# Kernel optimization log

Measured on AMD Instinct MI355X. Metric: run time of the kernel, lower is better.

## Reference

```python
import jax, jax.numpy as jnp
import numpy as np

B, S, H = 1, 2048, 4096
NH, NKV, D = 32, 8, 128
ROPE_THETA = 10000.0


def _rotate_half(x):
    half = x.shape[-1] // 2
    return jnp.concatenate([-x[..., half:], x[..., :half]], axis=-1)


def _rope_cos_sin(position_ids, dim, theta):
    inv_freq = 1.0 / (theta ** (jnp.arange(0, dim, 2, dtype=jnp.float32) / dim))  # [D/2]
    freqs = position_ids.astype(jnp.float32)[..., None] * inv_freq  # [B,S,D/2]
    emb = jnp.concatenate([freqs, freqs], axis=-1)  # [B,S,D]
    return jnp.cos(emb)[:, None], jnp.sin(emb)[:, None]  # [B,1,S,D]


def setup_inputs() -> dict:
    key = jax.random.key(0)
    k1, k2, k3 = jax.random.split(key, 3)
    hidden_states = jax.random.normal(k1, (B, S, H), dtype=jnp.float32)
    # fused QKV weight: columns = [NH*D | NKV*D | NKV*D]
    w_qkv = jax.random.normal(k2, (H, (NH + 2 * NKV) * D), dtype=jnp.float32) * (1.0 / np.sqrt(H))
    w_o = jax.random.normal(k3, (NH * D, H), dtype=jnp.float32) * (1.0 / np.sqrt(NH * D))
    attention_mask = jnp.tril(jnp.ones((S, S), dtype=bool))[None, None]  # causal [1,1,S,S]
    position_ids = jnp.arange(S, dtype=jnp.int64 if jax.config.jax_enable_x64 else jnp.int32)[None, :]
    return {"hidden_states": hidden_states, "w_qkv": w_qkv, "w_o": w_o,
            "attention_mask": attention_mask, "position_ids": position_ids}


def reference(hidden_states, w_qkv, w_o, attention_mask, position_ids):
    bsz, q_len, _ = hidden_states.shape
    qk_scale = 1.0 / np.sqrt(D)

    # fused QKV projection
    qkv = jnp.einsum('bsh,hc->bsc', hidden_states, w_qkv)
    q = qkv[..., : NH * D].reshape(bsz, q_len, NH, D).transpose(0, 2, 1, 3)        # [B,NH,S,D]
    k = qkv[..., NH * D: (NH + NKV) * D].reshape(bsz, q_len, NKV, D).transpose(0, 2, 1, 3)
    v = qkv[..., (NH + NKV) * D:].reshape(bsz, q_len, NKV, D).transpose(0, 2, 1, 3)

    # RoPE
    cos, sin = _rope_cos_sin(position_ids, D, ROPE_THETA)
    q = q * cos + _rotate_half(q) * sin
    k = k * cos + _rotate_half(k) * sin

    # GQA expand kv heads
    groups = NH // NKV
    k = jnp.repeat(k, groups, axis=1)  # [B,NH,S,D]
    v = jnp.repeat(v, groups, axis=1)

    # causal masked attention (eager path, matches scaled_qk + softmax(fp32))
    scores = jnp.einsum('bhqd,bhkd->bhqk', q, k) * qk_scale
    scores = jnp.where(attention_mask, scores, jnp.finfo(scores.dtype).min)
    probs = jax.nn.softmax(scores.astype(jnp.float32), axis=-1).astype(q.dtype)
    attn = jnp.einsum('bhqk,bhkd->bhqd', probs, v)  # [B,NH,S,D]

    # merge heads + output projection
    attn = attn.transpose(0, 2, 1, 3).reshape(bsz, q_len, NH * D)
    return jnp.einsum('bsd,dh->bsh', attn, w_o)
```

## Files before the change

kernel.cpp:

```cpp
#include <hip/hip_runtime.h>
#include <cstdint>
#include <cstddef>


#define DEV __device__ __forceinline__

typedef __attribute__((ext_vector_type(4))) float  f32x4;
typedef __attribute__((ext_vector_type(4))) short  short4v;
typedef __attribute__((ext_vector_type(8))) short  short8;
typedef __attribute__((ext_vector_type(8))) __bf16 bf16x8;

DEV short f32_to_bf16(float x) {
  union { float f; uint32_t u; } v; v.f = x;
  uint32_t r = v.u + 0x7fffu + ((v.u >> 16) & 1u);
  return (short)(r >> 16);
}

union frag_u { short4v h[2]; bf16x8 v; short s[8]; uint32_t u[4]; };
DEV bf16x8 comb(short4v lo, short4v hi) { frag_u u; u.h[0] = lo; u.h[1] = hi; return u.v; }

DEV uint32_t pack2bf_trunc(float a, float b) {
  union { float f; uint32_t u; } x, y; x.f = a; y.f = b;
  return (x.u >> 16) | (y.u & 0xFFFF0000u);
}

DEV f32x4 MFMA(bf16x8 a, bf16x8 b, f32x4 c) {
  return __builtin_amdgcn_mfma_f32_16x16x32_bf16(a, b, c, 0, 0, 0);
}

typedef __attribute__((address_space(1))) void* gas1p;
typedef __attribute__((address_space(3))) void* as3p;
DEV void gld16(const void* g, void* l) {
  __builtin_amdgcn_global_load_lds((gas1p)g, (as3p)l, 16, 0, 0);
}

#define VMCNT(n) asm volatile("s_waitcnt vmcnt(" #n ")" ::: "memory")


__global__ __launch_bounds__(256) void k_cvt_bf16(const float* __restrict__ x,
                                                  short* __restrict__ y, int n4) {
  int i = blockIdx.x * 256 + threadIdx.x;
  int stride = gridDim.x * 256;
  for (; i < n4; i += stride) {
    f32x4 v = ((const f32x4*)x)[i];
    short4v o;
    o[0] = f32_to_bf16(v[0]); o[1] = f32_to_bf16(v[1]);
    o[2] = f32_to_bf16(v[2]); o[3] = f32_to_bf16(v[3]);
    ((short4v*)y)[i] = o;
  }
}

__global__ __launch_bounds__(256) void k_transpose64(const float* __restrict__ src,
                                                     short* __restrict__ dst,
                                                     int R, int C, int stride) {
  __shared__ float tile[64][65];
  const int c0 = blockIdx.x * 64, r0 = blockIdx.y * 64;
  const int t = threadIdx.x;
  const int lr = t >> 4;
  const int lc = (t & 15) * 4;
  #pragma unroll
  for (int p = 0; p < 4; ++p) {
    const int r = p * 16 + lr;
    f32x4 v = *(const f32x4*)(src + (long)(r0 + r) * stride + c0 + lc);
    tile[r][lc] = v[0]; tile[r][lc + 1] = v[1]; tile[r][lc + 2] = v[2]; tile[r][lc + 3] = v[3];
  }
  __syncthreads();
  #pragma unroll
  for (int p = 0; p < 4; ++p) {
    const int c = p * 16 + lr;
    short4v o;
    o[0] = f32_to_bf16(tile[lc][c]);     o[1] = f32_to_bf16(tile[lc + 1][c]);
    o[2] = f32_to_bf16(tile[lc + 2][c]); o[3] = f32_to_bf16(tile[lc + 3][c]);
    *(short4v*)(dst + (long)(c0 + c) * R + r0 + lc) = o;
  }
}

__global__ __launch_bounds__(256) void k_vtrans64(const float* __restrict__ C1,
                                                  short* __restrict__ Vt) {
  __shared__ float tile[64][65];
  const int s0 = blockIdx.x * 64, d0 = blockIdx.y * 64, z = blockIdx.z;
  const int t = threadIdx.x;
  const int lr = t >> 4;
  const int lc = (t & 15) * 4;
  const float* src = C1 + 5120 + z * 128;
  #pragma unroll
  for (int p = 0; p < 4; ++p) {
    const int r = p * 16 + lr;
    f32x4 v = *(const f32x4*)(src + (long)(s0 + r) * 6144 + d0 + lc);
    tile[r][lc] = v[0]; tile[r][lc + 1] = v[1]; tile[r][lc + 2] = v[2]; tile[r][lc + 3] = v[3];
  }
  __syncthreads();
  short* dst = Vt + (long)z * 128 * 2048;
  #pragma unroll
  for (int p = 0; p < 4; ++p) {
    const int d = p * 16 + lr;
    short4v o;
    o[0] = f32_to_bf16(tile[lc][d]);     o[1] = f32_to_bf16(tile[lc + 1][d]);
    o[2] = f32_to_bf16(tile[lc + 2][d]); o[3] = f32_to_bf16(tile[lc + 3][d]);
    *(short4v*)(dst + (long)(d0 + d) * 2048 + s0 + lc) = o;
  }
}

__global__ __launch_bounds__(256) void k_rope_pack(const float* __restrict__ C1,
                                                   short* __restrict__ Qh,
                                                   short* __restrict__ Kh) {
  __shared__ float cs[64], sn[64];
  const int s = blockIdx.x, t = threadIdx.x;
  if (t < 64) {
    float inv = powf(10000.0f, -(float)t * (1.0f / 64.0f));
    float a = (float)s * inv;
    cs[t] = cosf(a);
    sn[t] = sinf(a);
  }
  __syncthreads();
  const float* row = C1 + (long)s * 6144;
  for (int i = t; i < 2048; i += 256) {
    int hh = i >> 6, j = i & 63;
    float c = cs[j], ss = sn[j];
    float x0 = row[hh * 128 + j], x1 = row[hh * 128 + j + 64];
    long o = ((long)hh * 2048 + s) * 128 + j;
    Qh[o]      = f32_to_bf16(x0 * c - x1 * ss);
    Qh[o + 64] = f32_to_bf16(x1 * c + x0 * ss);
  }
  for (int i = t; i < 512; i += 256) {
    int hh = i >> 6, j = i & 63;
    float c = cs[j], ss = sn[j];
    float x0 = row[4096 + hh * 128 + j], x1 = row[4096 + hh * 128 + j + 64];
    long o = ((long)hh * 2048 + s) * 128 + j;
    Kh[o]      = f32_to_bf16(x0 * c - x1 * ss);
    Kh[o + 64] = f32_to_bf16(x1 * c + x0 * ss);
  }
}


template<int MR>
DEV void gemm8p_engine(const short* __restrict__ A, const short* __restrict__ Bt,
                       float* __restrict__ Cp, int N, int K,
                       char* __restrict__ AsB, char* __restrict__ BsB) {
  constexpr int BM = MR * 32;
  const int tid = threadIdx.x;
  const int lane = tid & 63;
  const int w = tid >> 6;
  const int wm = w >> 2, wn = w & 3;
  const int wr = wm * (MR * 16);
  const int wc = wn * 64;
  const int g = lane >> 4, r16 = lane & 15;
  const long m0 = (long)blockIdx.y * BM;
  const long n0 = (long)blockIdx.x * 256;
  const int l8 = lane >> 3, l7 = lane & 7;
  const int sslot = l7 ^ l8;

  f32x4 acc[MR][4] = {};
  const int NT = K >> 6;

  auto stageA = [&](int h, int kt, int bufn) {
    #pragma unroll
    for (int s = 0; s < BM / 128; ++s) {
      const int rb = h * (BM / 2) + s * 64 + w * 8;
      gld16(A + (m0 + rb + l8) * (long)K + kt * 64 + sslot * 8,
            AsB + ((size_t)bufn * BM + rb) * 128);
    }
  };
  auto stageB = [&](int h, int kt, int bufn) {
    #pragma unroll
    for (int s = 0; s < 2; ++s) {
      const int rb = h * 128 + s * 64 + w * 8;
      gld16(Bt + (n0 + rb + l8) * (long)K + kt * 64 + sslot * 8,
            BsB + ((size_t)bufn * 256 + rb) * 128);
    }
  };

  bf16x8 a[MR / 2][2], b0[2][2], b1[2][2];

  #define LDA_HALF(h, buf) { _Pragma("unroll") for (int m = 0; m < MR/2; ++m) \
      _Pragma("unroll") for (int kk = 0; kk < 2; ++kk) { \
        const int row = wr + ((h) * (MR/2) + m) * 16 + r16; \
        const int slot = ((kk << 2) | g) ^ (r16 & 7); \
        a[m][kk] = *(const bf16x8*)(AsB + ((size_t)(buf) * BM + row) * 128 + slot * 16); } }
  #define LDB_HALF(dst, h, buf) { _Pragma("unroll") for (int n = 0; n < 2; ++n) \
      _Pragma("unroll") for (int kk = 0; kk < 2; ++kk) { \
        const int row = wc + ((h) * 2 + n) * 16 + r16; \
        const int slot = ((kk << 2) | g) ^ (r16 & 7); \
        dst[n][kk] = *(const bf16x8*)(BsB + ((size_t)(buf) * 256 + row) * 128 + slot * 16); } }
  #define QUADQ(mh, nh, bb) { __builtin_amdgcn_s_setprio(1); \
      _Pragma("unroll") for (int m = 0; m < MR/2; ++m) \
      _Pragma("unroll") for (int n = 0; n < 2; ++n) \
      _Pragma("unroll") for (int kk = 0; kk < 2; ++kk) \
        acc[(mh) * (MR/2) + m][(nh) * 2 + n] = \
          MFMA(a[m][kk], bb[n][kk], acc[(mh) * (MR/2) + m][(nh) * 2 + n]); \
      __builtin_amdgcn_s_setprio(0); }

  stageA(0, 0, 0); stageB(0, 0, 0); stageB(1, 0, 0); stageA(1, 0, 0);
  VMCNT(4);
  __builtin_amdgcn_s_barrier();

  for (int t = 0; t < NT - 1; ++t) {
    const int buf = t & 1, bufn = buf ^ 1, tn = t + 1;
    LDA_HALF(0, buf); LDB_HALF(b0, 0, buf);
    stageA(0, tn, bufn);
    __builtin_amdgcn_s_barrier();
    QUADQ(0, 0, b0);
    VMCNT(4);
    __builtin_amdgcn_s_barrier();
    LDB_HALF(b1, 1, buf);
    stageB(0, tn, bufn);
    __builtin_amdgcn_s_barrier();
    QUADQ(0, 1, b1);
    VMCNT(4);
    __builtin_amdgcn_s_barrier();
    LDA_HALF(1, buf);
    stageB(1, tn, bufn);
    __builtin_amdgcn_s_barrier();
    QUADQ(1, 1, b1);
    __builtin_amdgcn_s_barrier();
    stageA(1, tn, bufn);
    QUADQ(1, 0, b0);
    VMCNT(4);
    __builtin_amdgcn_s_barrier();
  }
  {
    const int buf = (NT - 1) & 1;
    LDA_HALF(0, buf); LDB_HALF(b0, 0, buf);
    __builtin_amdgcn_s_barrier();
    QUADQ(0, 0, b0);
    VMCNT(2);
    __builtin_amdgcn_s_barrier();
    LDB_HALF(b1, 1, buf);
    __builtin_amdgcn_s_barrier();
    QUADQ(0, 1, b1);
    VMCNT(0);
    __builtin_amdgcn_s_barrier();
    LDA_HALF(1, buf);
    __builtin_amdgcn_s_barrier();
    QUADQ(1, 1, b1);
    QUADQ(1, 0, b0);
  }
  #undef LDA_HALF
  #undef LDB_HALF
  #undef QUADQ

  #pragma unroll
  for (int m = 0; m < MR; ++m) {
    #pragma unroll
    for (int n = 0; n < 4; ++n) {
      const long col = n0 + wc + n * 16 + r16;
      #pragma unroll
      for (int j = 0; j < 4; ++j) {
        const long row = m0 + wr + m * 16 + g * 4 + j;
        Cp[row * N + col] = acc[m][n][j];
      }
    }
  }
}

__global__ __launch_bounds__(512, 2) void k_gemm1_8p(const short* __restrict__ A,
                                                     const short* __restrict__ Bt,
                                                     float* __restrict__ C, int N, int K) {
  __shared__ short As[2][256][64];
  __shared__ short Bs[2][256][64];
  gemm8p_engine<8>(A, Bt, C, N, K, (char*)&As[0][0][0], (char*)&Bs[0][0][0]);
}


template<int OUT_BF16>
__global__ __launch_bounds__(256, 2) void k_gemm128(const short* __restrict__ A,
                                                    const short* __restrict__ Bt,
                                                    void* __restrict__ Cp,
                                                    int M, int N, int K) {
  __shared__ short As[2][128][64];
  __shared__ short Bs[2][128][64];
  const int tid = threadIdx.x;
  const int lane = tid & 63;
  const int w = tid >> 6;
  const int wr = (w >> 1) * 64;
  const int wc = (w & 1) * 64;
  const int g = lane >> 4, r16 = lane & 15;
  const long m0 = (long)blockIdx.y * 128;
  const long n0 = (long)blockIdx.x * 128;
  const int l8 = lane >> 3, l7 = lane & 7;
  const int sslot = l7 ^ l8;

  f32x4 acc[4][4] = {};
  const int NT = K >> 6;

  auto stageTile = [&](int kt, int buf) {
    #pragma unroll
    for (int L = 0; L < 4; ++L) {
      const int rb = (w * 4 + L) * 8;
      gld16(A  + (m0 + rb + l8) * (long)K + kt * 64 + sslot * 8, (char*)&As[buf][rb][0]);
      gld16(Bt + (n0 + rb + l8) * (long)K + kt * 64 + sslot * 8, (char*)&Bs[buf][rb][0]);
    }
  };
  auto ldA = [&](int m, int kk, int buf) -> bf16x8 {
    const int row = wr + m * 16 + r16;
    const int slot = ((kk << 2) | g) ^ (r16 & 7);
    return *(const bf16x8*)((const char*)&As[buf][0][0] + row * 128 + slot * 16);
  };
  auto ldB = [&](int n, int kk, int buf) -> bf16x8 {
    const int row = wc + n * 16 + r16;
    const int slot = ((kk << 2) | g) ^ (r16 & 7);
    return *(const bf16x8*)((const char*)&Bs[buf][0][0] + row * 128 + slot * 16);
  };

  stageTile(0, 0);
  __syncthreads();

  for (int t = 0; t < NT; ++t) {
    const int buf = t & 1;
    if (t + 1 < NT) stageTile(t + 1, buf ^ 1);

    bf16x8 a[2][2], b[2][2];
    #pragma unroll
    for (int mh = 0; mh < 2; ++mh) {
      #pragma unroll
      for (int m = 0; m < 2; ++m)
        #pragma unroll
        for (int kk = 0; kk < 2; ++kk) a[m][kk] = ldA(mh * 2 + m, kk, buf);
      #pragma unroll
      for (int nh = 0; nh < 2; ++nh) {
        #pragma unroll
        for (int n = 0; n < 2; ++n)
          #pragma unroll
          for (int kk = 0; kk < 2; ++kk) b[n][kk] = ldB(nh * 2 + n, kk, buf);
        #pragma unroll
        for (int m = 0; m < 2; ++m)
          #pragma unroll
          for (int n = 0; n < 2; ++n)
            #pragma unroll
            for (int kk = 0; kk < 2; ++kk)
              acc[mh * 2 + m][nh * 2 + n] =
                MFMA(a[m][kk], b[n][kk], acc[mh * 2 + m][nh * 2 + n]);
      }
    }
    __syncthreads();
  }

  #pragma unroll
  for (int m = 0; m < 4; ++m) {
    #pragma unroll
    for (int n = 0; n < 4; ++n) {
      const long col = n0 + wc + n * 16 + r16;
      #pragma unroll
      for (int j = 0; j < 4; ++j) {
        const long row = m0 + wr + m * 16 + g * 4 + j;
        if (OUT_BF16) ((short*)Cp)[row * N + col] = f32_to_bf16(acc[m][n][j]);
        else          ((float*)Cp)[row * N + col] = acc[m][n][j];
      }
    }
  }
}


__global__ __launch_bounds__(256) void k_attn(const short* __restrict__ Qh,
                                              const short* __restrict__ Kh,
                                              const short* __restrict__ Vt,
                                              short* __restrict__ O) {
  __shared__ short Kl[64][136];
  __shared__ short Vl[128][72];
  const int h = blockIdx.x, qt = blockIdx.y, hk = h >> 2;
  const int tid = threadIdx.x, lane = tid & 63, w = tid >> 6;
  const int g = lane >> 4, r16 = lane & 15;
  const int q0 = qt * 64 + w * 16;
  const int q_glob = q0 + r16;

  bf16x8 qf[4];
  {
    const short* qb = Qh + ((long)h * 2048 + q0 + r16) * 128;
    #pragma unroll
    for (int c = 0; c < 4; ++c) {
      short4v lo = *(const short4v*)(qb + 32 * c + 4 * g);
      short4v hi = *(const short4v*)(qb + 32 * c + 16 + 4 * g);
      qf[c] = comb(lo, hi);
    }
  }
  const short* Kg = Kh + (long)hk * (2048 * 128);
  const short* Vg = Vt + (long)hk * (128 * 2048);

  f32x4 accO[8] = {};
  float mrun = -1e30f, lrun = 0.0f;

  short8 kpre[4], vpre[4];
  #pragma unroll
  for (int j = 0; j < 4; ++j) {
    const int n = tid + j * 256;
    kpre[j] = *(const short8*)(Kg + ((long)(n >> 4)) * 128 + (n & 15) * 8);
    vpre[j] = *(const short8*)(Vg + (long)(n >> 3) * 2048 + (n & 7) * 8);
  }

  for (int kt = 0; kt <= qt; ++kt) {
    #pragma unroll
    for (int j = 0; j < 4; ++j) {
      const int n = tid + j * 256;
      *(short8*)(&Kl[n >> 4][(n & 15) * 8]) = kpre[j];
      *(short8*)(&Vl[n >> 3][(n & 7) * 8]) = vpre[j];
    }
    __syncthreads();

    if (kt < qt) {
      const long koff = (long)(kt + 1) * 64;
      #pragma unroll
      for (int j = 0; j < 4; ++j) {
        const int n = tid + j * 256;
        kpre[j] = *(const short8*)(Kg + (koff + (n >> 4)) * 128 + (n & 15) * 8);
        vpre[j] = *(const short8*)(Vg + (long)(n >> 3) * 2048 + koff + (n & 7) * 8);
      }
    }

    f32x4 accS[4] = {};
    __builtin_amdgcn_s_setprio(1);
    #pragma unroll
    for (int kvf = 0; kvf < 4; ++kvf) {
      const short* kr = &Kl[kvf * 16 + r16][0];
      #pragma unroll
      for (int c = 0; c < 4; ++c) {
        short4v lo = *(const short4v*)(kr + 32 * c + 4 * g);
        short4v hi = *(const short4v*)(kr + 32 * c + 16 + 4 * g);
        accS[kvf] = MFMA(comb(lo, hi), qf[c], accS[kvf]);
      }
    }
    __builtin_amdgcn_s_setprio(0);

    float sc[4][4];
    #pragma unroll
    for (int kvf = 0; kvf < 4; ++kvf)
      #pragma unroll
      for (int r = 0; r < 4; ++r) sc[kvf][r] = accS[kvf][r] * 0.08838834764831845f;
    if (kt == qt) {
      #pragma unroll
      for (int kvf = 0; kvf < 4; ++kvf)
        #pragma unroll
        for (int r = 0; r < 4; ++r) {
          const int kvg = kt * 64 + kvf * 16 + g * 4 + r;
          if (kvg > q_glob) sc[kvf][r] = -1e30f;
        }
    }
    float rm[4];
    #pragma unroll
    for (int kvf = 0; kvf < 4; ++kvf)
      rm[kvf] = fmaxf(fmaxf(sc[kvf][0], sc[kvf][1]), fmaxf(sc[kvf][2], sc[kvf][3]));
    float mt = fmaxf(fmaxf(rm[0], rm[1]), fmaxf(rm[2], rm[3]));
    mt = fmaxf(mt, __shfl_xor(mt, 16));
    mt = fmaxf(mt, __shfl_xor(mt, 32));

    const bool nonew = __all(mt <= mrun);
    const float mnew = nonew ? mrun : fmaxf(mrun, mt);
    float pk[4];
    #pragma unroll
    for (int kvf = 0; kvf < 4; ++kvf) {
      #pragma unroll
      for (int r = 0; r < 4; ++r) sc[kvf][r] = __expf(sc[kvf][r] - mnew);
      pk[kvf] = (sc[kvf][0] + sc[kvf][1]) + (sc[kvf][2] + sc[kvf][3]);
    }
    float ps = (pk[0] + pk[1]) + (pk[2] + pk[3]);
    ps += __shfl_xor(ps, 16);
    ps += __shfl_xor(ps, 32);
    if (nonew) {
      lrun += ps;
    } else {
      const float scale = __expf(mrun - mnew);
      lrun = lrun * scale + ps;
      mrun = mnew;
      #pragma unroll
      for (int df = 0; df < 8; ++df)
        #pragma unroll
        for (int j = 0; j < 4; ++j) accO[df][j] *= scale;
    }

    frag_u p0, p1;
    p0.u[0] = pack2bf_trunc(sc[0][0], sc[0][1]);
    p0.u[1] = pack2bf_trunc(sc[0][2], sc[0][3]);
    p0.u[2] = pack2bf_trunc(sc[1][0], sc[1][1]);
    p0.u[3] = pack2bf_trunc(sc[1][2], sc[1][3]);
    p1.u[0] = pack2bf_trunc(sc[2][0], sc[2][1]);
    p1.u[1] = pack2bf_trunc(sc[2][2], sc[2][3]);
    p1.u[2] = pack2bf_trunc(sc[3][0], sc[3][1]);
    p1.u[3] = pack2bf_trunc(sc[3][2], sc[3][3]);

    __builtin_amdgcn_s_setprio(1);
    #pragma unroll
    for (int df = 0; df < 8; ++df) {
      const short* vr = &Vl[df * 16 + r16][0];
      short4v a0 = *(const short4v*)(vr + 4 * g);
      short4v a1 = *(const short4v*)(vr + 16 + 4 * g);
      short4v a2 = *(const short4v*)(vr + 32 + 4 * g);
      short4v a3 = *(const short4v*)(vr + 48 + 4 * g);
      accO[df] = MFMA(comb(a0, a1), p0.v, accO[df]);
      accO[df] = MFMA(comb(a2, a3), p1.v, accO[df]);
    }
    __builtin_amdgcn_s_setprio(0);
    __syncthreads();
  }

  const float invl = 1.0f / lrun;
  #pragma unroll
  for (int df = 0; df < 8; ++df) {
    const int d0 = df * 16 + g * 4;
    short4v o;
    #pragma unroll
    for (int j = 0; j < 4; ++j) o[j] = f32_to_bf16(accO[df][j] * invl);
    *(short4v*)(O + (long)q_glob * 4096 + h * 128 + d0) = o;
  }
}


extern "C" void kernel_launch(void* const* d_in, const int* in_sizes, int n_in,
                              void* d_out, int out_size, void* d_ws, size_t ws_size,
                              hipStream_t stream) {
  const float* hs   = (const float*)d_in[0];
  const float* wqkv = (const float*)d_in[1];
  const float* wo   = (const float*)d_in[2];

  const size_t OFF_HSB = 0;
  const size_t OFF_W1T = 16777216;
  const size_t OFF_WOT = 67108864;
  const size_t OFF_C1  = 100663296;
  const size_t OFF_KH  = 152043520;
  const size_t OFF_VT  = 156237824;
  if (ws_size < 160432128u) return;

  char* ws = (char*)d_ws;
  short* hsb = (short*)(ws + OFF_HSB);
  short* W1T = (short*)(ws + OFF_W1T);
  short* WoT = (short*)(ws + OFF_WOT);
  float* C1  = (float*)(ws + OFF_C1);
  short* Kh  = (short*)(ws + OFF_KH);
  short* Vt  = (short*)(ws + OFF_VT);
  short* Qh  = hsb;
  short* AO  = (short*)(ws + OFF_C1);

  k_cvt_bf16<<<2048, 256, 0, stream>>>(hs, hsb, 2048 * 4096 / 4);
  k_transpose64<<<dim3(96, 64), 256, 0, stream>>>(wqkv, W1T, 4096, 6144, 6144);
  k_transpose64<<<dim3(64, 64), 256, 0, stream>>>(wo, WoT, 4096, 4096, 4096);
  k_gemm1_8p<<<dim3(24, 8), 512, 0, stream>>>(hsb, W1T, C1, 6144, 4096);
  k_rope_pack<<<2048, 256, 0, stream>>>(C1, Qh, Kh);
  k_vtrans64<<<dim3(32, 2, 8), 256, 0, stream>>>(C1, Vt);
  k_attn<<<dim3(32, 32), 256, 0, stream>>>(Qh, Kh, Vt, AO);
  k_gemm128<0><<<dim3(32, 16), 256, 0, stream>>>(AO, WoT, (void*)d_out, 2048, 4096, 4096);
}
```

Before: 378.6 us.

## Enlarge attention query tile to 128 rows and interleave causal tile order

Each attention block now handles 128 query rows, with each wave processing two 16-row fragments, so every K/V tile staged in LDS is reused across twice as many queries. The grid is halved to 512 blocks, and q-tiles are remapped so heavy and light causal blocks alternate, which evens out load. Launch bounds request two blocks per CU. The aim is less K/V global and LDS traffic per query and fewer redundant fragment loads, at the cost of more accumulator registers and fewer blocks in flight.

```diff
diff --git a/kernel.cpp b/kernel.cpp
--- a/kernel.cpp
+++ b/kernel.cpp
@@ -351,33 +351,35 @@
 }
 
 
-__global__ __launch_bounds__(256) void k_attn(const short* __restrict__ Qh,
-                                              const short* __restrict__ Kh,
-                                              const short* __restrict__ Vt,
-                                              short* __restrict__ O) {
+__global__ __launch_bounds__(256, 2) void k_attn(const short* __restrict__ Qh,
+                                                 const short* __restrict__ Kh,
+                                                 const short* __restrict__ Vt,
+                                                 short* __restrict__ O) {
   __shared__ short Kl[64][136];
   __shared__ short Vl[128][72];
-  const int h = blockIdx.x, qt = blockIdx.y, hk = h >> 2;
+  const int h = blockIdx.x, by = blockIdx.y, hk = h >> 2;
+  const int qt = (by < 8) ? (2 * by) : (15 - 2 * (by - 8));
   const int tid = threadIdx.x, lane = tid & 63, w = tid >> 6;
   const int g = lane >> 4, r16 = lane & 15;
-  const int q0 = qt * 64 + w * 16;
-  const int q_glob = q0 + r16;
-
-  bf16x8 qf[4];
-  {
-    const short* qb = Qh + ((long)h * 2048 + q0 + r16) * 128;
+  const int q0w = qt * 128 + w * 32;
+
+  bf16x8 qf[2][4];
+  #pragma unroll
+  for (int qb = 0; qb < 2; ++qb) {
+    const short* qb_ptr = Qh + ((long)h * 2048 + q0w + qb * 16 + r16) * 128;
     #pragma unroll
     for (int c = 0; c < 4; ++c) {
-      short4v lo = *(const short4v*)(qb + 32 * c + 4 * g);
-      short4v hi = *(const short4v*)(qb + 32 * c + 16 + 4 * g);
-      qf[c] = comb(lo, hi);
+      short4v lo = *(const short4v*)(qb_ptr + 32 * c + 4 * g);
+      short4v hi = *(const short4v*)(qb_ptr + 32 * c + 16 + 4 * g);
+      qf[qb][c] = comb(lo, hi);
     }
   }
   const short* Kg = Kh + (long)hk * (2048 * 128);
   const short* Vg = Vt + (long)hk * (128 * 2048);
 
-  f32x4 accO[8] = {};
-  float mrun = -1e30f, lrun = 0.0f;
+  f32x4 accO[2][8] = {};
+  float mrun[2] = {-1e30f, -1e30f}, lrun[2] = {0.0f, 0.0f};
+  const int NTB = 2 * qt + 2;
 
   short8 kpre[4], vpre[4];
   #pragma unroll
@@ -387,7 +389,7 @@
     vpre[j] = *(const short8*)(Vg + (long)(n >> 3) * 2048 + (n & 7) * 8);
   }
 
-  for (int kt = 0; kt <= qt; ++kt) {
+  for (int kt = 0; kt < NTB; ++kt) {
     #pragma unroll
     for (int j = 0; j < 4; ++j) {
       const int n = tid + j * 256;
@@ -396,7 +398,7 @@
     }
     __syncthreads();
 
-    if (kt < qt) {
+    if (kt + 1 < NTB) {
       const long koff = (long)(kt + 1) * 64;
       #pragma unroll
       for (int j = 0; j < 4; ++j) {
@@ -406,99 +408,114 @@
       }
     }
 
-    f32x4 accS[4] = {};
-    __builtin_amdgcn_s_setprio(1);
-    #pragma unroll
-    for (int kvf = 0; kvf < 4; ++kvf) {
-      const short* kr = &Kl[kvf * 16 + r16][0];
-      #pragma unroll
-      for (int c = 0; c < 4; ++c) {
-        short4v lo = *(const short4v*)(kr + 32 * c + 4 * g);
-        short4v hi = *(const short4v*)(kr + 32 * c + 16 + 4 * g);
-        accS[kvf] = MFMA(comb(lo, hi), qf[c], accS[kvf]);
-      }
-    }
-    __builtin_amdgcn_s_setprio(0);
-
-    float sc[4][4];
-    #pragma unroll
-    for (int kvf = 0; kvf < 4; ++kvf)
-      #pragma unroll
-      for (int r = 0; r < 4; ++r) sc[kvf][r] = accS[kvf][r] * 0.08838834764831845f;
-    if (kt == qt) {
-      #pragma unroll
-      for (int kvf = 0; kvf < 4; ++kvf)
-        #pragma unroll
-        for (int r = 0; r < 4; ++r) {
-          const int kvg = kt * 64 + kvf * 16 + g * 4 + r;
-          if (kvg > q_glob) sc[kvf][r] = -1e30f;
+    if (kt * 64 <= q0w + 31) {
+      f32x4 accS[2][4] = {};
+      __builtin_amdgcn_s_setprio(1);
+      #pragma unroll
+      for (int kvf = 0; kvf < 4; ++kvf) {
+        const short* kr = &Kl[kvf * 16 + r16][0];
+        #pragma unroll
+        for (int c = 0; c < 4; ++c) {
+          short4v lo = *(const short4v*)(kr + 32 * c + 4 * g);
+          short4v hi = *(const short4v*)(kr + 32 * c + 16 + 4 * g);
+          bf16x8 af = comb(lo, hi);
+          accS[0][kvf] = MFMA(af, qf[0][c], accS[0][kvf]);
+          accS[1][kvf] = MFMA(af, qf[1][c], accS[1][kvf]);
         }
-    }
-    float rm[4];
-    #pragma unroll
-    for (int kvf = 0; kvf < 4; ++kvf)
-      rm[kvf] = fmaxf(fmaxf(sc[kvf][0], sc[kvf][1]), fmaxf(sc[kvf][2], sc[kvf][3]));
-    float mt = fmaxf(fmaxf(rm[0], rm[1]), fmaxf(rm[2], rm[3]));
-    mt = fmaxf(mt, __shfl_xor(mt, 16));
-    mt = fmaxf(mt, __shfl_xor(mt, 32));
-
-    const bool nonew = __all(mt <= mrun);
-    const float mnew = nonew ? mrun : fmaxf(mrun, mt);
-    float pk[4];
-    #pragma unroll
-    for (int kvf = 0; kvf < 4; ++kvf) {
-      #pragma unroll
-      for (int r = 0; r < 4; ++r) sc[kvf][r] = __expf(sc[kvf][r] - mnew);
-      pk[kvf] = (sc[kvf][0] + sc[kvf][1]) + (sc[kvf][2] + sc[kvf][3]);
-    }
-    float ps = (pk[0] + pk[1]) + (pk[2] + pk[3]);
-    ps += __shfl_xor(ps, 16);
-    ps += __shfl_xor(ps, 32);
-    if (nonew) {
-      lrun += ps;
-    } else {
-      const float scale = __expf(mrun - mnew);
-      lrun = lrun * scale + ps;
-      mrun = mnew;
-      #pragma unroll
-      for (int df = 0; df < 8; ++df)
-        #pragma unroll
-        for (int j = 0; j < 4; ++j) accO[df][j] *= scale;
-    }
-
-    frag_u p0, p1;
-    p0.u[0] = pack2bf_trunc(sc[0][0], sc[0][1]);
-    p0.u[1] = pack2bf_trunc(sc[0][2], sc[0][3]);
-    p0.u[2] = pack2bf_trunc(sc[1][0], sc[1][1]);
-    p0.u[3] = pack2bf_trunc(sc[1][2], sc[1][3]);
-    p1.u[0] = pack2bf_trunc(sc[2][0], sc[2][1]);
-    p1.u[1] = pack2bf_trunc(sc[2][2], sc[2][3]);
-    p1.u[2] = pack2bf_trunc(sc[3][0], sc[3][1]);
-    p1.u[3] = pack2bf_trunc(sc[3][2], sc[3][3]);
-
-    __builtin_amdgcn_s_setprio(1);
+      }
+      __builtin_amdgcn_s_setprio(0);
+
+      const bool diag = (kt * 64 + 63 > q0w);
+      frag_u p0[2], p1[2];
+      #pragma unroll
+      for (int qb = 0; qb < 2; ++qb) {
+        const int q_glob = q0w + qb * 16 + r16;
+        float sc[4][4];
+        #pragma unroll
+        for (int kvf = 0; kvf < 4; ++kvf)
+          #pragma unroll
+          for (int r = 0; r < 4; ++r) sc[kvf][r] = accS[qb][kvf][r] * 0.08838834764831845f;
+        if (diag) {
+          #pragma unroll
+          for (int kvf = 0; kvf < 4; ++kvf)
+            #pragma unroll
+            for (int r = 0; r < 4; ++r) {
+              const int kvg = kt * 64 + kvf * 16 + g * 4 + r;
+              if (kvg > q_glob) sc[kvf][r] = -1e30f;
+            }
+        }
+        float rm[4];
+        #pragma unroll
+        for (int kvf = 0; kvf < 4; ++kvf)
+          rm[kvf] = fmaxf(fmaxf(sc[kvf][0], sc[kvf][1]), fmaxf(sc[kvf][2], sc[kvf][3]));
+        float mt = fmaxf(fmaxf(rm[0], rm[1]), fmaxf(rm[2], rm[3]));
+        mt = fmaxf(mt, __shfl_xor(mt, 16));
+        mt = fmaxf(mt, __shfl_xor(mt, 32));
+
+        const bool nonew = __all(mt <= mrun[qb]);
+        const float mnew = nonew ? mrun[qb] : fmaxf(mrun[qb], mt);
+        float pk[4];
+        #pragma unroll
+        for (int kvf = 0; kvf < 4; ++kvf) {
+          #pragma unroll
+          for (int r = 0; r < 4; ++r) sc[kvf][r] = __expf(sc[kvf][r] - mnew);
+          pk[kvf] = (sc[kvf][0] + sc[kvf][1]) + (sc[kvf][2] + sc[kvf][3]);
+        }
+        float ps = (pk[0] + pk[1]) + (pk[2] + pk[3]);
+        ps += __shfl_xor(ps, 16);
+        ps += __shfl_xor(ps, 32);
+        if (nonew) {
+          lrun[qb] += ps;
+        } else {
+          const float scale = __expf(mrun[qb] - mnew);
+          lrun[qb] = lrun[qb] * scale + ps;
+          mrun[qb] = mnew;
+          #pragma unroll
+          for (int df = 0; df < 8; ++df)
+            #pragma unroll
+            for (int j = 0; j < 4; ++j) accO[qb][df][j] *= scale;
+        }
+        p0[qb].u[0] = pack2bf_trunc(sc[0][0], sc[0][1]);
+        p0[qb].u[1] = pack2bf_trunc(sc[0][2], sc[0][3]);
+        p0[qb].u[2] = pack2bf_trunc(sc[1][0], sc[1][1]);
+        p0[qb].u[3] = pack2bf_trunc(sc[1][2], sc[1][3]);
+        p1[qb].u[0] = pack2bf_trunc(sc[2][0], sc[2][1]);
+        p1[qb].u[1] = pack2bf_trunc(sc[2][2], sc[2][3]);
+        p1[qb].u[2] = pack2bf_trunc(sc[3][0], sc[3][1]);
+        p1[qb].u[3] = pack2bf_trunc(sc[3][2], sc[3][3]);
+      }
+
+      __builtin_amdgcn_s_setprio(1);
+      #pragma unroll
+      for (int df = 0; df < 8; ++df) {
+        const short* vr = &Vl[df * 16 + r16][0];
+        short4v a0 = *(const short4v*)(vr + 4 * g);
+        short4v a1 = *(const short4v*)(vr + 16 + 4 * g);
+        short4v a2 = *(const short4v*)(vr + 32 + 4 * g);
+        short4v a3 = *(const short4v*)(vr + 48 + 4 * g);
+        bf16x8 v01 = comb(a0, a1), v23 = comb(a2, a3);
+        accO[0][df] = MFMA(v01, p0[0].v, accO[0][df]);
+        accO[0][df] = MFMA(v23, p1[0].v, accO[0][df]);
+        accO[1][df] = MFMA(v01, p0[1].v, accO[1][df]);
+        accO[1][df] = MFMA(v23, p1[1].v, accO[1][df]);
+      }
+      __builtin_amdgcn_s_setprio(0);
+    }
+    __syncthreads();
+  }
+
+  #pragma unroll
+  for (int qb = 0; qb < 2; ++qb) {
+    const int q_glob = q0w + qb * 16 + r16;
+    const float invl = 1.0f / lrun[qb];
     #pragma unroll
     for (int df = 0; df < 8; ++df) {
-      const short* vr = &Vl[df * 16 + r16][0];
-      short4v a0 = *(const short4v*)(vr + 4 * g);
-      short4v a1 = *(const short4v*)(vr + 16 + 4 * g);
-      short4v a2 = *(const short4v*)(vr + 32 + 4 * g);
-      short4v a3 = *(const short4v*)(vr + 48 + 4 * g);
-      accO[df] = MFMA(comb(a0, a1), p0.v, accO[df]);
-      accO[df] = MFMA(comb(a2, a3), p1.v, accO[df]);
-    }
-    __builtin_amdgcn_s_setprio(0);
-    __syncthreads();
-  }
-
-  const float invl = 1.0f / lrun;
-  #pragma unroll
-  for (int df = 0; df < 8; ++df) {
-    const int d0 = df * 16 + g * 4;
-    short4v o;
-    #pragma unroll
-    for (int j = 0; j < 4; ++j) o[j] = f32_to_bf16(accO[df][j] * invl);
-    *(short4v*)(O + (long)q_glob * 4096 + h * 128 + d0) = o;
+      const int d0 = df * 16 + g * 4;
+      short4v o;
+      #pragma unroll
+      for (int j = 0; j < 4; ++j) o[j] = f32_to_bf16(accO[qb][df][j] * invl);
+      *(short4v*)(O + (long)q_glob * 4096 + h * 128 + d0) = o;
+    }
   }
 }
 
@@ -534,6 +551,6 @@
   k_gemm1_8p<<<dim3(24, 8), 512, 0, stream>>>(hsb, W1T, C1, 6144, 4096);
   k_rope_pack<<<2048, 256, 0, stream>>>(C1, Qh, Kh);
   k_vtrans64<<<dim3(32, 2, 8), 256, 0, stream>>>(C1, Vt);
-  k_attn<<<dim3(32, 32), 256, 0, stream>>>(Qh, Kh, Vt, AO);
+  k_attn<<<dim3(32, 16), 256, 0, stream>>>(Qh, Kh, Vt, AO);
   k_gemm128<0><<<dim3(32, 16), 256, 0, stream>>>(AO, WoT, (void*)d_out, 2048, 4096, 4096);
 }
```

Result: faster. 350.1 us (median of 2 runs) (-7.5%).
